# Kernel tuning notes

Hardware: AMD Instinct MI355X
Metric: run time of the kernel (lower is better)

Reference implementation:

```python
import jax, jax.numpy as jnp
import numpy as np

B, FDIM, T, N, TOPK = 64, 80, 400, 5, 2
EPS = 1e-5


def conv2d(x, w, stride, pad):
    return jax.lax.conv_general_dilated(
        x, w, window_strides=stride,
        padding=[(pad, pad), (pad, pad)],
        dimension_numbers=('NCHW', 'OIHW', 'NCHW'))


def bn2d(x, g, b):
    # eval-mode BatchNorm2d with running_mean=0, running_var=1
    s = g / jnp.sqrt(1.0 + EPS)
    return x * s[None, :, None, None] + b[None, :, None, None]


def gelu(x):
    return jax.nn.gelu(x, approximate=False)  # torch nn.GELU default (erf)


def setup_inputs() -> dict:
    key = jax.random.key(0)
    ks = jax.random.split(key, 12)

    def rn(k, shape, scale=0.05):
        return jax.random.normal(k, shape, dtype=jnp.float32) * scale

    return {
        'x': rn(ks[0], (B, 1, FDIM, T, N), 1.0),
        'total': rn(ks[1], (B, 1, FDIM, 5 * T), 1.0),
        'gw1': rn(ks[2], (32, 1, 5, 15)),
        'g1': jnp.ones((32,), jnp.float32), 'b1': jnp.zeros((32,), jnp.float32),
        'gw2': rn(ks[3], (64, 32, 5, 15)),
        'g2': jnp.ones((64,), jnp.float32), 'b2': jnp.zeros((64,), jnp.float32),
        'gw3': rn(ks[4], (128, 64, 5, 15)),
        'g3': jnp.ones((128,), jnp.float32), 'b3': jnp.zeros((128,), jnp.float32),
        'gw4': rn(ks[5], (256, 128, 5, 15)),
        'g4': jnp.ones((256,), jnp.float32), 'b4': jnp.zeros((256,), jnp.float32),
        'fw1': rn(ks[6], (32, 256)), 'fb1': jnp.zeros((32,), jnp.float32),
        'g1d': jnp.ones((32,), jnp.float32), 'b1d': jnp.zeros((32,), jnp.float32),
        'fw2': rn(ks[7], (5, 32)), 'fb2': jnp.zeros((5,), jnp.float32),
        'cw1': rn(ks[8], (64, 1, 7, 14)),
    }


def reference(x, total, gw1, g1, b1, gw2, g2, b2, gw3, g3, b3, gw4, g4, b4,
              fw1, fb1, g1d, b1d, fw2, fb2, cw1):
    h = gelu(bn2d(conv2d(total, gw1, (2, 4), 2), g1, b1))
    h = gelu(bn2d(conv2d(h, gw2, (2, 4), 2), g2, b2))
    h = gelu(bn2d(conv2d(h, gw3, (2, 4), 2), g3, b3))
    h = gelu(bn2d(conv2d(h, gw4, (2, 4), 2), g4, b4))
    h = h.mean(axis=(2, 3))                      # AdaptiveAvgPool2d((1,1)) + Flatten -> [B,256]
    h = gelu(h @ fw1.T + fb1)                    # Linear(256,32) + GELU
    h = h * (g1d / jnp.sqrt(1.0 + EPS)) + b1d    # eval-mode BatchNorm1d(32)
    routing_weights = h @ fw2.T + fb2            # Linear(32,5) -> [B,5]

    # ---- top-k routing ----
    probs = jax.nn.softmax(routing_weights, axis=1)
    _, sel = jax.lax.top_k(probs, TOPK)          # [B,2]
    sel = jnp.sort(sel, axis=1)
    mask = jnp.transpose(jax.nn.one_hot(sel, N, dtype=x.dtype), (0, 2, 1))  # [B,5,2]

    # ---- one-hot einsum gather + reshape + stem conv ----
    gated = jnp.einsum('bcftn,bns->bcfts', x, mask)      # [B,1,80,T,2]
    gated = gated.reshape(-1, 1, FDIM, TOPK * gated.shape[3])  # [B,1,80,2T]
    out = conv2d(gated, cw1, (2, 2), 3)                  # [B,64,40,397]
    return out, routing_weights
```

## Files before the change

### kernel.cpp

```cpp
#include <hip/hip_runtime.h>
#include <hip/hip_bf16.h>

#define DEV __device__ __forceinline__

typedef __attribute__((ext_vector_type(8))) short short8_t;
typedef __attribute__((ext_vector_type(4))) float f32x4;

DEV float gelu_erf(float x) { return 0.5f * x * (1.0f + erff(x * 0.70710678118654752440f)); }

DEV ushort f2bf(float v) { __hip_bfloat16 h = __float2bfloat16(v); return *(ushort*)&h; }

__global__ void prep_k(const float* __restrict__ gw1, const float* __restrict__ gw2,
                       const float* __restrict__ gw3, const float* __restrict__ gw4,
                       const float* __restrict__ cw1,
                       ushort* __restrict__ wp1, ushort* __restrict__ wp2,
                       ushort* __restrict__ wp3, ushort* __restrict__ w4p,
                       ushort* __restrict__ wp5, ushort* __restrict__ zp)
{
    int idx = blockIdx.x * blockDim.x + threadIdx.x;
    if (idx < 2457600) {
        int kp = idx % 9600, oc = idx / 9600;
        int ic = kp & 127, kc = kp >> 7;
        w4p[idx] = f2bf(gw4[((size_t)oc * 128 + ic) * 75 + kc]);
        return;
    }
    idx -= 2457600;
    if (idx < 614400) {
        int ic = idx % 64, t = idx / 64;
        int oc = t % 128, kc = t / 128;
        wp3[idx] = f2bf(gw3[((size_t)oc * 64 + ic) * 75 + kc]);
        return;
    }
    idx -= 614400;
    if (idx < 153600) {
        int ic = idx % 32, t = idx / 32;
        int oc = t % 64, kc = t / 64;
        wp2[idx] = f2bf(gw2[((size_t)oc * 32 + ic) * 75 + kc]);
        return;
    }
    idx -= 153600;
    if (idx < 8192) {
        int oc = idx >> 7, k = idx & 127;
        int kh = k >> 4, t = k & 15;
        int a = t >> 1, c = t & 1, kw = 2 * a + c - 1;
        float v = (kh < 7 && kw >= 0 && kw < 14) ? cw1[oc * 98 + kh * 14 + kw] : 0.f;
        wp5[idx] = f2bf(v);
        return;
    }
    idx -= 8192;
    if (idx < 3072) {
        int oc = idx / 96, k = idx % 96;
        int kh = k >> 4, kw = k & 15;
        float v = (kh < 5 && kw < 15) ? gw1[oc * 75 + kh * 15 + kw] : 0.f;
        wp1[idx] = f2bf(v);
        return;
    }
    idx -= 3072;
    zp[idx] = 0;
}

template <int M_BLK, int NOC, int NCH, int NWM, int NWN, int ST, bool F32IN, bool BNG>
__global__ __launch_bounds__(64 * NWM * NWN) void convmm1_k(
    const void* __restrict__ in_, const ushort* __restrict__ wp,
    const float* __restrict__ gamma, const float* __restrict__ beta,
    void* __restrict__ out_,
    int IH, int IWE, int OH, int OW, int NOWT, int PH)
{
    constexpr int NT = 64 * NWM * NWN;
    constexpr int NR = 2 * NCH;
    constexpr int SPAN = (M_BLK - 1) * ST + 16;
    constexpr int SSTR = ((SPAN + 7) & ~7) + 2;
    constexpr int STAGE_B = NR * SSTR * 2;
    constexpr int TILE_B = BNG ? (M_BLK * NOC * 2) : (NOC * M_BLK * 4);
    constexpr int SMEM_B = STAGE_B > TILE_B ? STAGE_B : TILE_B;
    __shared__ __align__(16) char smem[SMEM_B];
    ushort* stg = (ushort*)smem;

    int bid = blockIdx.x;
    const int owt = bid % NOWT; bid /= NOWT;
    const int oh = bid % OH;
    const int b  = bid / OH;
    const int ow0 = owt * M_BLK;
    const int tid = threadIdx.x;
    const int w = tid >> 6, l = tid & 63;
    const int wn = w % NWN, wm = w / NWN;
    const int m_wave = wm * 32, n_wave = wn * 32;
    const int lc = l & 15, lr = l >> 4;

    if (F32IN) {
        for (int u = tid; u < NR * SPAN; u += NT) {
            int r = u / SPAN, e = u - r * SPAN;
            int ih = oh * 2 - PH + r;
            int iw = ow0 * ST - 2 + e;
            float v = 0.f;
            if ((unsigned)ih < (unsigned)IH && (unsigned)iw < (unsigned)IWE)
                v = ((const float*)in_)[((size_t)b * IH + ih) * IWE + iw];
            stg[r * SSTR + e] = f2bf(v);
        }
    } else {
        constexpr int SPANU = SPAN / 2;
        for (int u = tid; u < NR * SPANU; u += NT) {
            int r = u / SPANU, e = u - r * SPANU;
            int ih = oh * 2 - PH + r;
            int iu = ow0 - 2 + e;
            uint v = 0;
            if ((unsigned)ih < (unsigned)IH && (unsigned)iu < (unsigned)IWE)
                v = ((const uint*)in_)[((size_t)b * IH + ih) * IWE + iu];
            *(uint*)&stg[r * SSTR + e * 2] = v;
        }
    }

    short8_t bfr[NCH][2];
    {
        const ushort* wb = wp + (size_t)(n_wave + lc) * (NCH * 32) + lr * 8;
#pragma unroll
        for (int cc = 0; cc < NCH; ++cc)
#pragma unroll
            for (int nj = 0; nj < 2; ++nj)
                bfr[cc][nj] = *(const short8_t*)(wb + (size_t)nj * 16 * (NCH * 32) + cc * 32);
    }

    __syncthreads();

    f32x4 acc[2][2];
#pragma unroll
    for (int i = 0; i < 2; ++i)
#pragma unroll
        for (int j = 0; j < 2; ++j) acc[i][j] = (f32x4){0.f, 0.f, 0.f, 0.f};

#pragma unroll
    for (int cc = 0; cc < NCH; ++cc) {
        const int kh = 2 * cc + (lr >> 1);
        const uint* lrow = (const uint*)&stg[kh * SSTR];
        short8_t a[2];
#pragma unroll
        for (int mi = 0; mi < 2; ++mi) {
            const int m = m_wave + mi * 16 + lc;
            const int half = (m * ST + (lr & 1) * 8) >> 1;
            union { uint u[4]; short8_t s; } av;
            av.u[0] = lrow[half];
            av.u[1] = lrow[half + 1];
            av.u[2] = lrow[half + 2];
            av.u[3] = lrow[half + 3];
            a[mi] = av.s;
        }
#pragma unroll
        for (int mi = 0; mi < 2; ++mi)
#pragma unroll
            for (int nj = 0; nj < 2; ++nj)
                acc[mi][nj] = __builtin_amdgcn_mfma_f32_16x16x32_bf16(a[mi], bfr[cc][nj], acc[mi][nj], 0, 0, 0);
    }

    __syncthreads();

    if (BNG) {
        ushort* tile = (ushort*)smem;
#pragma unroll
        for (int nj = 0; nj < 2; ++nj) {
            const int n = n_wave + nj * 16 + lc;
            const float s = gamma[n] * rsqrtf(1.0f + 1e-5f);
            const float bb = beta[n];
#pragma unroll
            for (int mi = 0; mi < 2; ++mi)
#pragma unroll
                for (int r = 0; r < 4; ++r) {
                    const int m = m_wave + mi * 16 + lr * 4 + r;
                    float y = gelu_erf(fmaf(acc[mi][nj][r], s, bb));
                    tile[m * NOC + n] = f2bf(y);
                }
        }
        __syncthreads();
        const int mv = min(M_BLK, OW - ow0);
        uint* dst = (uint*)((ushort*)out_ + (((size_t)b * OH + oh) * OW + ow0) * NOC);
        const uint* src = (const uint*)tile;
        for (int idx = tid; idx < mv * NOC / 2; idx += NT) dst[idx] = src[idx];
    } else {
        float* tile = (float*)smem;
#pragma unroll
        for (int nj = 0; nj < 2; ++nj) {
            const int n = n_wave + nj * 16 + lc;
#pragma unroll
            for (int mi = 0; mi < 2; ++mi)
#pragma unroll
                for (int r = 0; r < 4; ++r) {
                    const int m = m_wave + mi * 16 + lr * 4 + r;
                    tile[n * M_BLK + m] = acc[mi][nj][r];
                }
        }
        __syncthreads();
        const int mv = min(M_BLK, OW - ow0);
        float* outb = (float*)out_ + ((size_t)b * NOC * OH + oh) * OW + ow0;
        for (int idx = tid; idx < NOC * mv; idx += NT) {
            int oc = idx / mv, j = idx - oc * mv;
            outb[(size_t)oc * OH * OW + j] = tile[oc * M_BLK + j];
        }
    }
}

template <int M_BLK, int OC, int ICT, int NICC, int NWM, int NWN, int UNR>
__global__ __launch_bounds__(64 * NWM * NWN) void convmm_k(
    const ushort* __restrict__ in, const ushort* __restrict__ wp,
    const float* __restrict__ gamma, const float* __restrict__ beta,
    ushort* __restrict__ out,
    int IH, int IW, int OH, int OW, int NOWT)
{
    constexpr int KH = 5, KW = 15, SW = 4;
    constexpr int MI = M_BLK / (16 * NWM);
    constexpr int NJ = OC / (16 * NWN);
    constexpr int SPAN = (M_BLK - 1) * SW + KW;
    constexpr int ICB = ICT * 2;
    constexpr int NSL = ICT / 8;
    constexpr int KEYM = NSL - 1;
    constexpr int NT = 64 * NWM * NWN;
    constexpr int NUNITS = SPAN * NSL;
    constexpr int NLD = (NUNITS + NT - 1) / NT;

    __shared__ __align__(16) ushort Abuf[SPAN * ICT];

    int bid = blockIdx.x;
    const int owt = bid % NOWT; bid /= NOWT;
    const int oh  = bid % OH;
    const int b   = bid / OH;
    const int ow0 = owt * M_BLK;
    const int tid = threadIdx.x;
    const int w = tid >> 6, l = tid & 63;
    const int wn = w % NWN, wm = w / NWN;
    const int m_wave = wm * (16 * MI), n_wave = wn * (16 * NJ);
    const int lc = l & 15, lr = l >> 4;

    const int ih0 = oh * 2 - 2;
    const int iw0 = ow0 * SW - 2;
    const ushort* inb = in + (size_t)b * IH * IW * ICT;

    int up[NLD], usl[NLD], uoff[NLD];
    bool uv[NLD];
#pragma unroll
    for (int i = 0; i < NLD; ++i) {
        int u = tid + i * NT;
        uv[i] = u < NUNITS;
        int uu = uv[i] ? u : 0;
        up[i] = uu / NSL;
        usl[i] = uu - up[i] * NSL;
        uoff[i] = up[i] * ICB + ((usl[i] ^ ((up[i] >> 2) & KEYM)) << 4);
    }

    uint4 rg[NLD];
    auto prefetch = [&](int kh) {
        const int ih = ih0 + kh;
        const bool rowok = (unsigned)ih < (unsigned)IH;
        const ushort* src = inb + (size_t)ih * IW * ICT;
#pragma unroll
        for (int i = 0; i < NLD; ++i) {
            int iw = iw0 + up[i];
            uint4 v = {0u, 0u, 0u, 0u};
            if (rowok && uv[i] && (unsigned)iw < (unsigned)IW)
                v = *(const uint4*)(src + (size_t)iw * ICT + usl[i] * 8);
            rg[i] = v;
        }
    };
    auto writestage = [&]() {
#pragma unroll
        for (int i = 0; i < NLD; ++i)
            if (uv[i]) *(uint4*)((char*)Abuf + uoff[i]) = rg[i];
    };

    f32x4 acc[MI][NJ];
#pragma unroll
    for (int i = 0; i < MI; ++i)
#pragma unroll
        for (int j = 0; j < NJ; ++j) acc[i][j] = (f32x4){0.f, 0.f, 0.f, 0.f};

    prefetch(0);
    writestage();
    __syncthreads();

#pragma unroll 1
    for (int kh = 0; kh < KH; ++kh) {
        if (kh + 1 < KH) prefetch(kh + 1);
        const char* buf = (const char*)Abuf;
        const ushort* wkh = wp + (size_t)(kh * KW) * OC * ICT + (size_t)(n_wave + lc) * ICT + lr * 8;
#pragma unroll UNR
        for (int kw = 0; kw < KW; ++kw) {
#pragma unroll
            for (int icc = 0; icc < NICC; ++icc) {
                short8_t a[MI], bf[NJ];
#pragma unroll
                for (int mi = 0; mi < MI; ++mi) {
                    const int r = m_wave + mi * 16 + lc;
                    const int p = SW * r + kw;
                    const int sl = icc * 4 + lr;
                    a[mi] = *(const short8_t*)(buf + p * ICB + ((sl ^ ((p >> 2) & KEYM)) << 4));
                }
                const ushort* wb = wkh + (size_t)kw * OC * ICT + icc * 32;
#pragma unroll
                for (int nj = 0; nj < NJ; ++nj)
                    bf[nj] = *(const short8_t*)(wb + (size_t)nj * 16 * ICT);
#pragma unroll
                for (int mi = 0; mi < MI; ++mi)
#pragma unroll
                    for (int nj = 0; nj < NJ; ++nj)
                        acc[mi][nj] = __builtin_amdgcn_mfma_f32_16x16x32_bf16(a[mi], bf[nj], acc[mi][nj], 0, 0, 0);
            }
        }
        if (kh + 1 < KH) {
            __syncthreads();
            writestage();
            __syncthreads();
        }
    }

    ushort* outb = out + ((size_t)b * OH + oh) * OW * OC;
#pragma unroll
    for (int nj = 0; nj < NJ; ++nj) {
        const int n = n_wave + nj * 16 + lc;
        const float s = gamma[n] * rsqrtf(1.0f + 1e-5f);
        const float bb = beta[n];
#pragma unroll
        for (int mi = 0; mi < MI; ++mi) {
#pragma unroll
            for (int r = 0; r < 4; ++r) {
                const int m = m_wave + mi * 16 + lr * 4 + r;
                const int ow = ow0 + m;
                if (ow < OW) {
                    float y = gelu_erf(fmaf(acc[mi][nj][r], s, bb));
                    outb[(size_t)ow * OC + n] = f2bf(y);
                }
            }
        }
    }
}

__global__ __launch_bounds__(256) void gemm4_k(
    const ushort* __restrict__ h3, const ushort* __restrict__ Bw,
    const ushort* __restrict__ zp, float* __restrict__ part)
{
    __shared__ __align__(16) ushort Al[3][64 * 64];
    __shared__ __align__(16) ushort Bl[3][64 * 64];
    int bid = blockIdx.x;
    const int ks = bid & 3;
    const int nt = (bid >> 2) & 3;
    const int mt = bid >> 4;
    const int m0 = mt * 64, n0 = nt * 64;
    const int k0 = (ks * 150) / 4, k1 = ((ks + 1) * 150) / 4;
    const int tid = threadIdx.x;
    const int w = tid >> 6, l = tid & 63;
    const int wr = (w >> 1) * 32, wc = (w & 1) * 32;
    const int lc = l & 15, lr = l >> 4;

    int ihb[2], iwb[2], bb[2], sspo[2];
    const ushort* gbrow[2];
#pragma unroll
    for (int i = 0; i < 2; ++i) {
        int u = tid + i * 256;
        int row = u >> 3, sl = u & 7;
        int rg = m0 + row;
        int b_ = rg / 25, p = rg - b_ * 25;
        int oh = p / 5, ow = p - oh * 5;
        bb[i] = b_;
        ihb[i] = oh * 2 - 2;
        iwb[i] = ow * 4 - 2;
        sspo[i] = (sl ^ (row & 7)) * 8;
        gbrow[i] = Bw + (size_t)(n0 + row) * 9600 + sspo[i];
    }

    auto stage = [&](int kc, int buf) {
        const int kcp = kc >> 1;
        const int kh = kcp / 15, kw = kcp - kh * 15;
        const int ice = (kc & 1) * 64;
#pragma unroll
        for (int i = 0; i < 2; ++i) {
            const int ih = ihb[i] + kh, iw = iwb[i] + kw;
            const ushort* srcA = ((unsigned)ih < 10u && (unsigned)iw < 28u)
                ? h3 + ((((size_t)bb[i] * 10 + ih) * 28 + iw) << 7) + ice + sspo[i]
                : zp;
            __builtin_amdgcn_global_load_lds(srcA, &Al[buf][(tid + i * 256) * 8], 16, 0, 0);
            __builtin_amdgcn_global_load_lds(gbrow[i] + kc * 64, &Bl[buf][(tid + i * 256) * 8], 16, 0, 0);
        }
    };

    f32x4 acc[2][2];
#pragma unroll
    for (int i = 0; i < 2; ++i)
#pragma unroll
        for (int j = 0; j < 2; ++j) acc[i][j] = (f32x4){0.f, 0.f, 0.f, 0.f};

    auto compute = [&](int buf) {
        short8_t a[2][2], bq[2][2];
#pragma unroll
        for (int mi = 0; mi < 2; ++mi)
#pragma unroll
            for (int ks_ = 0; ks_ < 2; ++ks_) {
                const int row = wr + mi * 16 + lc;
                const int sl = (ks_ * 4 + lr) ^ (row & 7);
                a[mi][ks_] = *(const short8_t*)&Al[buf][row * 64 + sl * 8];
            }
#pragma unroll
        for (int nj = 0; nj < 2; ++nj)
#pragma unroll
            for (int ks_ = 0; ks_ < 2; ++ks_) {
                const int row = wc + nj * 16 + lc;
                const int sl = (ks_ * 4 + lr) ^ (row & 7);
                bq[nj][ks_] = *(const short8_t*)&Bl[buf][row * 64 + sl * 8];
            }
#pragma unroll
        for (int ks_ = 0; ks_ < 2; ++ks_)
#pragma unroll
            for (int mi = 0; mi < 2; ++mi)
#pragma unroll
                for (int nj = 0; nj < 2; ++nj)
                    acc[mi][nj] = __builtin_amdgcn_mfma_f32_16x16x32_bf16(a[mi][ks_], bq[nj][ks_], acc[mi][nj], 0, 0, 0);
    };

    stage(k0, 0); stage(k0 + 1, 1); stage(k0 + 2, 2);
    int buf = 0;
#pragma unroll 1
    for (int kc = k0; kc < k1 - 3; ++kc) {
        asm volatile("s_waitcnt vmcnt(8)" ::: "memory");
        __syncthreads();
        compute(buf);
        __syncthreads();
        stage(kc + 3, buf);
        buf = (buf == 2) ? 0 : buf + 1;
    }
    asm volatile("s_waitcnt vmcnt(8)" ::: "memory"); __syncthreads(); compute(buf); buf = (buf == 2) ? 0 : buf + 1;
    asm volatile("s_waitcnt vmcnt(4)" ::: "memory"); __syncthreads(); compute(buf); buf = (buf == 2) ? 0 : buf + 1;
    asm volatile("s_waitcnt vmcnt(0)" ::: "memory"); __syncthreads(); compute(buf);

    float* dst = part + (size_t)ks * 409600;
#pragma unroll
    for (int mi = 0; mi < 2; ++mi)
#pragma unroll
        for (int nj = 0; nj < 2; ++nj) {
            const int n = n0 + wc + 16 * nj + lc;
#pragma unroll
            for (int r = 0; r < 4; ++r) {
                const int m = m0 + wr + 16 * mi + 4 * lr + r;
                dst[(size_t)m * 256 + n] = acc[mi][nj][r];
            }
        }
}

__global__ void route_k(const float* __restrict__ part,
                        const float* __restrict__ g4, const float* __restrict__ b4,
                        const float* __restrict__ fw1, const float* __restrict__ fb1,
                        const float* __restrict__ g1d, const float* __restrict__ b1d,
                        const float* __restrict__ fw2, const float* __restrict__ fb2,
                        float* __restrict__ rw_out, int* __restrict__ sel_out)
{
    __shared__ float pooled[256];
    __shared__ float hmid[32];
    __shared__ float rwv[5];
    const int b = blockIdx.x, c = threadIdx.x;
    const float s4 = g4[c] * rsqrtf(1.0f + 1e-5f);
    const float bb4 = b4[c];
    const float* p = part + (size_t)b * 25 * 256 + c;
    float sum = 0.f;
#pragma unroll
    for (int i = 0; i < 25; ++i) {
        float v = p[i * 256] + p[409600 + i * 256] + p[819200 + i * 256] + p[1228800 + i * 256];
        sum += gelu_erf(fmaf(v, s4, bb4));
    }
    pooled[c] = sum * (1.0f / 25.0f);
    __syncthreads();
    if (c < 32) {
        float a = fb1[c];
        const float* wr = fw1 + c * 256;
        for (int i = 0; i < 256; ++i) a += pooled[i] * wr[i];
        a = gelu_erf(a);
        a = a * (g1d[c] * rsqrtf(1.0f + 1e-5f)) + b1d[c];
        hmid[c] = a;
    }
    __syncthreads();
    if (c < 5) {
        float a = fb2[c];
        const float* wr = fw2 + c * 32;
#pragma unroll
        for (int i = 0; i < 32; ++i) a += hmid[i] * wr[i];
        rwv[c] = a;
        rw_out[b * 5 + c] = a;
    }
    __syncthreads();
    if (c == 0) {
        int i1 = 0;
        for (int i = 1; i < 5; ++i) if (rwv[i] > rwv[i1]) i1 = i;
        int i2 = -1;
        for (int i = 0; i < 5; ++i) {
            if (i == i1) continue;
            if (i2 < 0 || rwv[i] > rwv[i2]) i2 = i;
        }
        sel_out[b * 2]     = i1 < i2 ? i1 : i2;
        sel_out[b * 2 + 1] = i1 < i2 ? i2 : i1;
    }
}

__global__ void gather_k(const float* __restrict__ x, const int* __restrict__ sel,
                         uint* __restrict__ gated)
{
    const int idx = blockIdx.x * blockDim.x + threadIdx.x;
    const int b = idx / 32000;
    const int s0 = sel[b * 2], s1 = sel[b * 2 + 1];
    const float* xp = x + (size_t)idx * 5;
    __hip_bfloat16 h0 = __float2bfloat16(xp[s0]);
    __hip_bfloat16 h1 = __float2bfloat16(xp[s1]);
    gated[idx] = (uint)*(ushort*)&h0 | ((uint)*(ushort*)&h1 << 16);
}

extern "C" void kernel_launch(void* const* d_in, const int* in_sizes, int n_in,
                              void* d_out, int out_size, void* d_ws, size_t ws_size,
                              hipStream_t stream)
{
    const float* x     = (const float*)d_in[0];
    const float* total = (const float*)d_in[1];
    const float* gw1 = (const float*)d_in[2];
    const float* g1  = (const float*)d_in[3];
    const float* b1  = (const float*)d_in[4];
    const float* gw2 = (const float*)d_in[5];
    const float* g2  = (const float*)d_in[6];
    const float* b2  = (const float*)d_in[7];
    const float* gw3 = (const float*)d_in[8];
    const float* g3  = (const float*)d_in[9];
    const float* b3  = (const float*)d_in[10];
    const float* gw4 = (const float*)d_in[11];
    const float* g4  = (const float*)d_in[12];
    const float* b4  = (const float*)d_in[13];
    const float* fw1 = (const float*)d_in[14];
    const float* fb1 = (const float*)d_in[15];
    const float* g1d = (const float*)d_in[16];
    const float* b1d = (const float*)d_in[17];
    const float* fw2 = (const float*)d_in[18];
    const float* fb2 = (const float*)d_in[19];
    const float* cw1 = (const float*)d_in[20];

    char* ws = (char*)d_ws;
    size_t off = 0;
    auto alloc = [&](size_t bytes) { void* p = ws + off; off = (off + bytes + 255) & ~(size_t)255; return p; };
    ushort* h1n = (ushort*)alloc((size_t)40796160 * 2);
    ushort* h2n = (ushort*)alloc((size_t)9994240 * 2);
    ushort* h3n = (ushort*)alloc((size_t)2293760 * 2);
    float* part  = (float*)alloc((size_t)4 * 409600 * 4);
    int*   sel   = (int*)alloc(512);
    uint*  gated = (uint*)alloc((size_t)2048000 * 4);
    ushort* wp1 = (ushort*)alloc((size_t)3072 * 2);
    ushort* wp2 = (ushort*)alloc((size_t)153600 * 2);
    ushort* wp3 = (ushort*)alloc((size_t)614400 * 2);
    ushort* w4p = (ushort*)alloc((size_t)2457600 * 2);
    ushort* wp5 = (ushort*)alloc((size_t)8192 * 2);
    ushort* zp  = (ushort*)alloc(512);

    float* outc = (float*)d_out;
    float* rw   = outc + (size_t)65044480;

    prep_k<<<12645, 256, 0, stream>>>(gw1, gw2, gw3, gw4, cw1, wp1, wp2, wp3, w4p, wp5, zp);

    convmm1_k<128, 32, 3, 4, 1, 4, true, true><<<64 * 40 * 4, 256, 0, stream>>>(
        total, wp1, g1, b1, h1n, 80, 2000, 40, 498, 4, 2);

    convmm_k<128, 64, 32, 1, 2, 2, 5><<<64 * 20, 256, 0, stream>>>(
        h1n, wp2, g2, b2, h2n, 40, 498, 20, 122, 1);

    convmm_k<32, 128, 64, 2, 1, 4, 5><<<64 * 10, 256, 0, stream>>>(
        h2n, wp3, g3, b3, h3n, 20, 122, 10, 28, 1);

    gemm4_k<<<400, 256, 0, stream>>>(h3n, w4p, zp, part);

    route_k<<<64, 256, 0, stream>>>(part, g4, b4, fw1, fb1, g1d, b1d, fw2, fb2, rw, sel);
    gather_k<<<8000, 256, 0, stream>>>(x, sel, gated);

    convmm1_k<64, 64, 4, 2, 2, 2, false, false><<<64 * 40 * 7, 256, 0, stream>>>(
        gated, wp5, nullptr, nullptr, outc, 80, 400, 40, 397, 7, 3);
}
```

Measured before the change: 457.8 us.

## Vectorize staging loads and gather, add XCD-aware block swizzle

The input staging loops in convmm1_k now load aligned 16-byte groups (float4/uint4) with a scalar fallback at edges. This needs a padded shared-memory row stride and a small read offset (HOFF) to line up with the aligned start. gather_k now handles four output elements per thread using float4 loads and select chains instead of indexed scalar loads. Both conv kernels remap block IDs so neighbouring tiles share an XCD's L2 cache. The changes aim to cut global load instruction count and improve cache locality, but add edge-handling complexity and assume the grid size divides evenly by 8.

Result: faster. 423.7 us (median of 2 runs) (-7.5%).

```diff
diff --git a/kernel.cpp b/kernel.cpp
--- a/kernel.cpp
+++ b/kernel.cpp
@@ -7,8 +7,12 @@
 typedef __attribute__((ext_vector_type(4))) float f32x4;
 
 DEV float gelu_erf(float x) { return 0.5f * x * (1.0f + erff(x * 0.70710678118654752440f)); }
-
 DEV ushort f2bf(float v) { __hip_bfloat16 h = __float2bfloat16(v); return *(ushort*)&h; }
+
+DEV int xcd_swz(int bid, int nwg) {
+    int q = nwg >> 3;
+    return (bid & 7) * q + (bid >> 3);
+}
 
 __global__ void prep_k(const float* __restrict__ gw1, const float* __restrict__ gw2,
                        const float* __restrict__ gw3, const float* __restrict__ gw4,
@@ -69,14 +73,15 @@
     constexpr int NT = 64 * NWM * NWN;
     constexpr int NR = 2 * NCH;
     constexpr int SPAN = (M_BLK - 1) * ST + 16;
-    constexpr int SSTR = ((SPAN + 7) & ~7) + 2;
+    constexpr int SSTR = ((SPAN + 16 + 7) & ~7) + 8;
     constexpr int STAGE_B = NR * SSTR * 2;
     constexpr int TILE_B = BNG ? (M_BLK * NOC * 2) : (NOC * M_BLK * 4);
     constexpr int SMEM_B = STAGE_B > TILE_B ? STAGE_B : TILE_B;
+    constexpr int HOFF = F32IN ? 1 : 2;
     __shared__ __align__(16) char smem[SMEM_B];
     ushort* stg = (ushort*)smem;
 
-    int bid = blockIdx.x;
+    int bid = xcd_swz(blockIdx.x, gridDim.x);
     const int owt = bid % NOWT; bid /= NOWT;
     const int oh = bid % OH;
     const int b  = bid / OH;
@@ -88,25 +93,52 @@
     const int lc = l & 15, lr = l >> 4;
 
     if (F32IN) {
-        for (int u = tid; u < NR * SPAN; u += NT) {
-            int r = u / SPAN, e = u - r * SPAN;
+        constexpr int NG = (SPAN + 6) / 4 + 1;
+        const int iwb_al = (ow0 * ST - 2) & ~3;
+        const float* inf = (const float*)in_;
+        for (int u = tid; u < NR * NG; u += NT) {
+            int r = u / NG, gi = u - r * NG;
             int ih = oh * 2 - PH + r;
-            int iw = ow0 * ST - 2 + e;
-            float v = 0.f;
-            if ((unsigned)ih < (unsigned)IH && (unsigned)iw < (unsigned)IWE)
-                v = ((const float*)in_)[((size_t)b * IH + ih) * IWE + iw];
-            stg[r * SSTR + e] = f2bf(v);
+            int iw4 = iwb_al + gi * 4;
+            int q = gi * 4;
+            bool rowok = (unsigned)ih < (unsigned)IH;
+            if (rowok && iw4 >= 0 && iw4 + 3 < IWE) {
+                float4 v = *(const float4*)&inf[((size_t)b * IH + ih) * IWE + iw4];
+                ushort4 h;
+                h.x = f2bf(v.x); h.y = f2bf(v.y); h.z = f2bf(v.z); h.w = f2bf(v.w);
+                *(ushort4*)&stg[r * SSTR + q] = h;
+            } else {
+#pragma unroll
+                for (int j = 0; j < 4; ++j) {
+                    int iw = iw4 + j;
+                    float v = (rowok && (unsigned)iw < (unsigned)IWE)
+                        ? inf[((size_t)b * IH + ih) * IWE + iw] : 0.f;
+                    stg[r * SSTR + q + j] = f2bf(v);
+                }
+            }
         }
     } else {
         constexpr int SPANU = SPAN / 2;
-        for (int u = tid; u < NR * SPANU; u += NT) {
-            int r = u / SPANU, e = u - r * SPANU;
+        constexpr int NGU = (SPANU + 6) / 4 + 1;
+        const int iub_al = (ow0 - 2) & ~3;
+        const uint* inu = (const uint*)in_;
+        for (int u = tid; u < NR * NGU; u += NT) {
+            int r = u / NGU, gi = u - r * NGU;
             int ih = oh * 2 - PH + r;
-            int iu = ow0 - 2 + e;
-            uint v = 0;
-            if ((unsigned)ih < (unsigned)IH && (unsigned)iu < (unsigned)IWE)
-                v = ((const uint*)in_)[((size_t)b * IH + ih) * IWE + iu];
-            *(uint*)&stg[r * SSTR + e * 2] = v;
+            int iu4 = iub_al + gi * 4;
+            bool rowok = (unsigned)ih < (unsigned)IH;
+            if (rowok && iu4 >= 0 && iu4 + 3 < IWE) {
+                uint4 v = *(const uint4*)&inu[((size_t)b * IH + ih) * IWE + iu4];
+                *(uint4*)&stg[r * SSTR + gi * 8] = v;
+            } else {
+#pragma unroll
+                for (int j = 0; j < 4; ++j) {
+                    int iu = iu4 + j;
+                    uint v = (rowok && (unsigned)iu < (unsigned)IWE)
+                        ? inu[((size_t)b * IH + ih) * IWE + iu] : 0u;
+                    *(uint*)&stg[r * SSTR + gi * 8 + j * 2] = v;
+                }
+            }
         }
     }
 
@@ -136,7 +168,7 @@
 #pragma unroll
         for (int mi = 0; mi < 2; ++mi) {
             const int m = m_wave + mi * 16 + lc;
-            const int half = (m * ST + (lr & 1) * 8) >> 1;
+            const int half = ((m * ST + (lr & 1) * 8) >> 1) + HOFF;
             union { uint u[4]; short8_t s; } av;
             av.u[0] = lrow[half];
             av.u[1] = lrow[half + 1];
@@ -217,7 +249,7 @@
 
     __shared__ __align__(16) ushort Abuf[SPAN * ICT];
 
-    int bid = blockIdx.x;
+    int bid = xcd_swz(blockIdx.x, gridDim.x);
     const int owt = bid % NOWT; bid /= NOWT;
     const int oh  = bid % OH;
     const int b   = bid / OH;
@@ -494,15 +526,39 @@
 }
 
 __global__ void gather_k(const float* __restrict__ x, const int* __restrict__ sel,
-                         uint* __restrict__ gated)
+                         uint4* __restrict__ gated)
 {
-    const int idx = blockIdx.x * blockDim.x + threadIdx.x;
-    const int b = idx / 32000;
+    const int g = blockIdx.x * blockDim.x + threadIdx.x;
+    const int idx0 = g * 4;
+    const int b = idx0 / 32000;
     const int s0 = sel[b * 2], s1 = sel[b * 2 + 1];
-    const float* xp = x + (size_t)idx * 5;
-    __hip_bfloat16 h0 = __float2bfloat16(xp[s0]);
-    __hip_bfloat16 h1 = __float2bfloat16(xp[s1]);
-    gated[idx] = (uint)*(ushort*)&h0 | ((uint)*(ushort*)&h1 << 16);
+    const float* xp = x + (size_t)idx0 * 5;
+    float4 v0 = *(const float4*)(xp);
+    float4 v1 = *(const float4*)(xp + 4);
+    float4 v2 = *(const float4*)(xp + 8);
+    float4 v3 = *(const float4*)(xp + 12);
+    float4 v4 = *(const float4*)(xp + 16);
+    float vals[5][4];
+    vals[0][0] = v0.x; vals[1][0] = v0.y; vals[2][0] = v0.z; vals[3][0] = v0.w; vals[4][0] = v1.x;
+    vals[0][1] = v1.y; vals[1][1] = v1.z; vals[2][1] = v1.w; vals[3][1] = v2.x; vals[4][1] = v2.y;
+    vals[0][2] = v2.z; vals[1][2] = v2.w; vals[2][2] = v3.x; vals[3][2] = v3.y; vals[4][2] = v3.z;
+    vals[0][3] = v3.w; vals[1][3] = v4.x; vals[2][3] = v4.y; vals[3][3] = v4.z; vals[4][3] = v4.w;
+    uint out[4];
+#pragma unroll
+    for (int j = 0; j < 4; ++j) {
+        float lo = vals[0][j];
+        lo = (s0 == 1) ? vals[1][j] : lo;
+        lo = (s0 == 2) ? vals[2][j] : lo;
+        lo = (s0 == 3) ? vals[3][j] : lo;
+        lo = (s0 == 4) ? vals[4][j] : lo;
+        float hi = vals[0][j];
+        hi = (s1 == 1) ? vals[1][j] : hi;
+        hi = (s1 == 2) ? vals[2][j] : hi;
+        hi = (s1 == 3) ? vals[3][j] : hi;
+        hi = (s1 == 4) ? vals[4][j] : hi;
+        out[j] = (uint)f2bf(lo) | ((uint)f2bf(hi) << 16);
+    }
+    gated[g] = (uint4){out[0], out[1], out[2], out[3]};
 }
 
 extern "C" void kernel_launch(void* const* d_in, const int* in_sizes, int n_in,
@@ -564,7 +620,8 @@
     gemm4_k<<<400, 256, 0, stream>>>(h3n, w4p, zp, part);
 
     route_k<<<64, 256, 0, stream>>>(part, g4, b4, fw1, fb1, g1d, b1d, fw2, fb2, rw, sel);
-    gather_k<<<8000, 256, 0, stream>>>(x, sel, gated);
+
+    gather_k<<<2000, 256, 0, stream>>>(x, sel, (uint4*)gated);
 
     convmm1_k<64, 64, 4, 2, 2, 2, false, false><<<64 * 40 * 7, 256, 0, stream>>>(
         gated, wp5, nullptr, nullptr, outc, 80, 400, 40, 397, 7, 3);
```
